# Kernel tuning notes

Measured on AMD Instinct MI355X. Metric: run time of the kernel, lower is better.

The kernel has to match this reference:

```python
import jax, jax.numpy as jnp
import numpy as np

TEMPERATURE = 0.1
B, T, D = 8, 1024, 1024
NEG_INF = -1e30

def setup_inputs() -> dict:
    key = jax.random.key(0)
    k1, k2, k3 = jax.random.split(key, 3)
    features = jax.random.normal(k1, (B, T, D), dtype=jnp.float32)
    masks = jax.random.bernoulli(k2, 0.05, (B, 1, T, T)).astype(jnp.float32)
    input_coords_length = jax.random.randint(k3, (B,), T // 2, T - 1)  # int32
    return {"features": features, "masks": masks, "input_coords_length": input_coords_length}


def _sup_con_loss(feat, mask, L):
    # feat: [T, D], mask: [T, T] float, L: scalar int valid length (slice [:L, :L])
    Tn = feat.shape[0]
    dt = feat.dtype
    vr = jnp.arange(Tn) < L                              # valid rows/cols [T]
    valid2d = (vr[:, None] & vr[None, :]).astype(dt)     # [T, T]
    dot = jnp.matmul(feat, feat.T) / TEMPERATURE         # [T, T]
    dot = jnp.where(vr[None, :], dot, NEG_INF)           # exclude padded cols from max
    logits = dot - jax.lax.stop_gradient(jnp.max(dot, axis=-1, keepdims=True))
    logits_mask = (1.0 - jnp.eye(Tn, dtype=dt)) * valid2d  # off-diagonal, in-slice
    exp_logits = jnp.exp(logits) * logits_mask
    m = mask * valid2d
    # negative_mask = 1-mask; entries < 1 zeroed (binary mask -> indicator of mask==0)
    neg = 1.0 - m
    neg = jnp.where(neg < 1.0, 0.0, neg) * valid2d
    # positive_mask = mask with entries > 0 set to 1
    pos = jnp.where(m > 0, 1.0, m)
    neg_denom = jnp.sum(exp_logits * neg, axis=-1, keepdims=True)
    pos_denom = jax.lax.stop_gradient(jnp.sum(exp_logits * pos, axis=-1, keepdims=True))
    log_prob = logits - jnp.log(neg_denom + pos_denom + 1e-6)
    m2 = m * logits_mask
    mean_log_prob_pos = (m2 * log_prob).sum(-1) / (m2.sum(-1) + 1e-6)  # [T]
    # mean over the L valid rows only (matches .mean() on the sliced tensor)
    return -jnp.sum(jnp.where(vr, mean_log_prob_pos, 0.0)) / L.astype(dt)


def _is_valid(mask, L):
    # valid sample iff sliced mask differs from eye(L) with [0,0]=0
    Tn = mask.shape[0]
    vr = jnp.arange(Tn) < L
    valid2d = (vr[:, None] & vr[None, :]).astype(mask.dtype)
    sanity = jnp.eye(Tn, dtype=mask.dtype).at[0, 0].set(0.0) * valid2d
    return jnp.any((mask * valid2d) != sanity)


def reference(features, masks, input_coords_length):
    L = input_coords_length + 1                      # [B]
    mask0 = masks[:, 0]                              # [B, T, T] (num_layers asserted == 1)
    losses = jax.vmap(_sup_con_loss)(features, mask0, L)   # [B]
    valid = jax.vmap(_is_valid)(mask0, L)                  # [B] bool
    vbs = jnp.maximum(jnp.sum(valid.astype(features.dtype)), 1.0)
    return jnp.sum(losses) / vbs
```

## Files before the change

kernel.cpp:

```cpp
#include <hip/hip_runtime.h>
#include <hip/hip_bf16.h>
#include <stdint.h>

#define T_DIM 1024
#define B_DIM 8

typedef __attribute__((ext_vector_type(8))) short short8;
typedef __attribute__((ext_vector_type(4))) float f32x4;

__device__ inline void gll16(const void* g, void* l) {
  __builtin_amdgcn_global_load_lds((__attribute__((address_space(1))) void*)g,
                                   (__attribute__((address_space(3))) void*)l,
                                   16, 0, 0);
}

__global__ __launch_bounds__(256) void convert_kernel(const float* __restrict__ F,
                                                      __hip_bfloat16* __restrict__ Fb) {
  const int t = blockIdx.x * 256 + threadIdx.x;
  const float4 v = ((const float4*)F)[t];
  union { __hip_bfloat16 h[4]; uint64_t u; } p;
  p.h[0] = __float2bfloat16(v.x);
  p.h[1] = __float2bfloat16(v.y);
  p.h[2] = __float2bfloat16(v.z);
  p.h[3] = __float2bfloat16(v.w);
  ((uint64_t*)Fb)[t] = p.u;
}

__global__ __launch_bounds__(512) void fused_kernel(const __hip_bfloat16* __restrict__ Fb,
                                                    const float* __restrict__ M,
                                                    const int* __restrict__ icl,
                                                    float* __restrict__ part) {
  const int b  = blockIdx.z;
  const int rt = blockIdx.y;
  const int ct = blockIdx.x;
  const int L  = icl[b] + 1;
  if (rt * 128 >= L || ct * 128 >= L) return;

  __shared__ __hip_bfloat16 As[2][4096];
  __shared__ __hip_bfloat16 Bs[2][4096];
  __shared__ float rp_m[128][4], rp_d[128][4], rp_s[128][4], rp_c[128][4], rp_b[128][4];

  const __hip_bfloat16* F = Fb + ((size_t)b << 20);
  const int tid  = threadIdx.x;
  const int lane = tid & 63;
  const int wave = tid >> 6;
  const int wrow = (wave >> 2) * 64;
  const int wcol = (wave & 3) * 32;
  const int row0 = rt * 128;
  const int col0 = ct * 128;
  const bool diag = (rt == ct);

  const int fr = lane & 15;
  const int q  = lane >> 4;
  const int fk = q * 8;

  const int sr = tid >> 2;
  const int sk = (tid & 3) * 8;

  f32x4 acc[4][2];
#pragma unroll
  for (int i = 0; i < 4; i++)
#pragma unroll
    for (int j = 0; j < 2; j++) acc[i][j] = (f32x4){0.f, 0.f, 0.f, 0.f};

  for (int k0 = 0; k0 < T_DIM; k0 += 64) {
    __syncthreads();
    gll16(F + (size_t)(row0 + sr) * T_DIM + k0 + sk,      &As[0][tid * 8]);
    gll16(F + (size_t)(row0 + sr) * T_DIM + k0 + 32 + sk, &As[1][tid * 8]);
    if (!diag) {
      gll16(F + (size_t)(col0 + sr) * T_DIM + k0 + sk,      &Bs[0][tid * 8]);
      gll16(F + (size_t)(col0 + sr) * T_DIM + k0 + 32 + sk, &Bs[1][tid * 8]);
    }
    __syncthreads();
#pragma unroll
    for (int kk = 0; kk < 2; kk++) {
      const __hip_bfloat16* Ab = As[kk];
      const __hip_bfloat16* Bb = diag ? As[kk] : Bs[kk];
      short8 af[4], bfr[2];
#pragma unroll
      for (int t = 0; t < 4; t++)
        af[t] = *(const short8*)(Ab + (wrow + t * 16 + fr) * 32 + fk);
#pragma unroll
      for (int j = 0; j < 2; j++)
        bfr[j] = *(const short8*)(Bb + (wcol + j * 16 + fr) * 32 + fk);
#pragma unroll
      for (int ti = 0; ti < 4; ti++)
#pragma unroll
        for (int tj = 0; tj < 2; tj++)
          acc[ti][tj] = __builtin_amdgcn_mfma_f32_16x16x32_bf16(af[ti], bfr[tj], acc[ti][tj], 0, 0, 0);
    }
  }

  const float* Mb = M + ((size_t)b << 20);
  const int gc0 = col0 + wcol + fr;
  const int gc1 = gc0 + 16;
#pragma unroll
  for (int ti = 0; ti < 4; ti++) {
#pragma unroll
    for (int r = 0; r < 4; r++) {
      const int lrow = wrow + ti * 16 + q * 4 + r;
      const int grow = row0 + lrow;
      const float s0 = (gc0 < L) ? acc[ti][0][r] * 10.0f : -1e30f;
      const float s1 = (gc1 < L) ? acc[ti][1][r] * 10.0f : -1e30f;
      float m = fmaxf(s0, s1);
#pragma unroll
      for (int d = 1; d < 16; d <<= 1) m = fmaxf(m, __shfl_xor(m, d, 64));
      float den = 0.f, msum = 0.f, cnt = 0.f, badf = 0.f;
      if (gc0 < L) {
        const float mk = Mb[(size_t)grow * T_DIM + gc0];
        if (gc0 != grow) { den += __expf(s0 - m); msum += mk * s0; cnt += mk; }
        const float sane = (gc0 == grow && grow != 0) ? 1.f : 0.f;
        badf = fmaxf(badf, (mk != sane) ? 1.f : 0.f);
      }
      if (gc1 < L) {
        const float mk = Mb[(size_t)grow * T_DIM + gc1];
        if (gc1 != grow) { den += __expf(s1 - m); msum += mk * s1; cnt += mk; }
        const float sane = (gc1 == grow && grow != 0) ? 1.f : 0.f;
        badf = fmaxf(badf, (mk != sane) ? 1.f : 0.f);
      }
#pragma unroll
      for (int d = 1; d < 16; d <<= 1) {
        den  += __shfl_xor(den, d, 64);
        msum += __shfl_xor(msum, d, 64);
        cnt  += __shfl_xor(cnt, d, 64);
        badf  = fmaxf(badf, __shfl_xor(badf, d, 64));
      }
      if (fr == 0) {
        const int slot = wave & 3;
        rp_m[lrow][slot] = m;   rp_d[lrow][slot] = den;
        rp_s[lrow][slot] = msum; rp_c[lrow][slot] = cnt;
        rp_b[lrow][slot] = badf;
      }
    }
  }
  __syncthreads();

  if (tid < 128) {
    float m = -1e30f;
#pragma unroll
    for (int s = 0; s < 4; s++) m = fmaxf(m, rp_m[tid][s]);
    float den = 0.f, msum = 0.f, cnt = 0.f, badf = 0.f;
#pragma unroll
    for (int s = 0; s < 4; s++) {
      den  += rp_d[tid][s] * __expf(rp_m[tid][s] - m);
      msum += rp_s[tid][s];
      cnt  += rp_c[tid][s];
      badf  = fmaxf(badf, rp_b[tid][s]);
    }
    float* p = part + ((((size_t)b * 1024 + row0 + tid) * 8) + ct) * 5;
    p[0] = m; p[1] = den; p[2] = msum; p[3] = cnt; p[4] = badf;
  }
}

__global__ __launch_bounds__(256) void reduce_kernel(const float* __restrict__ part,
                                                     const int* __restrict__ icl,
                                                     float* __restrict__ blk_sum,
                                                     int* __restrict__ blk_bad) {
  const int blk = blockIdx.x;
  const int row = blk * 256 + threadIdx.x;
  const int b = row >> 10;
  const int i = row & 1023;
  const int L = icl[b] + 1;
  float rv = 0.f;
  int bad = 0;
  if (i < L) {
    const float* p = part + (size_t)row * 40;
    const int ns = (L + 127) >> 7;
    float m = -1e30f;
    for (int s = 0; s < ns; s++) m = fmaxf(m, p[s * 5 + 0]);
    float den = 0.f, msum = 0.f, cnt = 0.f, badf = 0.f;
    for (int s = 0; s < ns; s++) {
      den  += p[s * 5 + 1] * __expf(p[s * 5 + 0] - m);
      msum += p[s * 5 + 2];
      cnt  += p[s * 5 + 3];
      badf  = fmaxf(badf, p[s * 5 + 4]);
    }
    const float A = msum - cnt * m;
    const float mlpp = (A - cnt * __logf(den + 1e-6f)) / (cnt + 1e-6f);
    rv = -mlpp / (float)L;
    bad = badf > 0.f ? 1 : 0;
  }
  const int tid  = threadIdx.x;
  const int lane = tid & 63;
  const int wave = tid >> 6;
  for (int o = 32; o > 0; o >>= 1) rv += __shfl_down(rv, o, 64);
  const int wbad = (__ballot(bad) != 0ull) ? 1 : 0;
  __shared__ float sred[4];
  __shared__ int bred[4];
  if (lane == 0) { sred[wave] = rv; bred[wave] = wbad; }
  __syncthreads();
  if (tid == 0) {
    blk_sum[blk] = sred[0] + sred[1] + sred[2] + sred[3];
    blk_bad[blk] = bred[0] | bred[1] | bred[2] | bred[3];
  }
}

__global__ __launch_bounds__(64) void final_kernel(const float* __restrict__ blk_sum,
                                                   const int* __restrict__ blk_bad,
                                                   float* __restrict__ out) {
  const int tid = threadIdx.x;
  float v = (tid < 32) ? blk_sum[tid] : 0.f;
  for (int o = 32; o > 0; o >>= 1) v += __shfl_down(v, o, 64);
  if (tid == 0) {
    int vcount = 0;
    for (int bb = 0; bb < B_DIM; bb++) {
      const int any = blk_bad[bb * 4] | blk_bad[bb * 4 + 1] |
                      blk_bad[bb * 4 + 2] | blk_bad[bb * 4 + 3];
      vcount += any ? 1 : 0;
    }
    out[0] = v / fmaxf((float)vcount, 1.0f);
  }
}

extern "C" void kernel_launch(void* const* d_in, const int* in_sizes, int n_in,
                              void* d_out, int out_size, void* d_ws, size_t ws_size,
                              hipStream_t stream) {
  const float* feat = (const float*)d_in[0];
  const float* mask = (const float*)d_in[1];
  const int*   icl  = (const int*)d_in[2];
  float* out = (float*)d_out;

  char* ws = (char*)d_ws;
  __hip_bfloat16* Fb = (__hip_bfloat16*)ws;
  float* part    = (float*)(ws + (16u << 20));
  float* blk_sum = (float*)(ws + (18u << 20));
  int*   blk_bad = (int*)(ws + (18u << 20) + 512);

  convert_kernel<<<dim3(8192), dim3(256), 0, stream>>>(feat, Fb);
  fused_kernel<<<dim3(8, 8, 8), dim3(512), 0, stream>>>(Fb, mask, icl, part);
  reduce_kernel<<<dim3(32), dim3(256), 0, stream>>>(part, icl, blk_sum, blk_bad);
  final_kernel<<<dim3(1), dim3(64), 0, stream>>>(blk_sum, blk_bad, out);
}
```

Before: 138.5 us.

## Double K-step per barrier, XOR-swizzle LDS, alias epilogue scratch, prefetch mask loads

Each loop iteration now loads 128 K-elements into four 32-wide LDS slabs, which halves the number of barrier pairs. An XOR swizzle on the 16-byte chunk index is applied both to the global source address and to the fragment read offset, to cut LDS bank conflicts on fragment reads. The reduction scratch now aliases the tile buffers in a single 64KB shared array, which needs an extra barrier after the main loop. The mask loads for each 16-row group are issued together before the reduction math so their global latency overlaps. The larger LDS footprint may lower occupancy.

```diff
diff --git a/kernel.cpp b/kernel.cpp
--- a/kernel.cpp
+++ b/kernel.cpp
@@ -36,9 +36,15 @@
   const int L  = icl[b] + 1;
   if (rt * 128 >= L || ct * 128 >= L) return;
 
-  __shared__ __hip_bfloat16 As[2][4096];
-  __shared__ __hip_bfloat16 Bs[2][4096];
-  __shared__ float rp_m[128][4], rp_d[128][4], rp_s[128][4], rp_c[128][4], rp_b[128][4];
+  __shared__ char smem[65536];
+  __hip_bfloat16* As = (__hip_bfloat16*)smem;
+  __hip_bfloat16* Bs = (__hip_bfloat16*)(smem + 32768);
+  float* rp = (float*)smem;
+  float* rp_m = rp;
+  float* rp_d = rp + 512;
+  float* rp_s = rp + 1024;
+  float* rp_c = rp + 1536;
+  float* rp_b = rp + 2048;
 
   const __hip_bfloat16* F = Fb + ((size_t)b << 20);
   const int tid  = threadIdx.x;
@@ -52,10 +58,10 @@
 
   const int fr = lane & 15;
   const int q  = lane >> 4;
-  const int fk = q * 8;
-
-  const int sr = tid >> 2;
-  const int sk = (tid & 3) * 8;
+  const int sl8 = (q ^ ((fr >> 1) & 3)) * 8;
+
+  const int srow = tid >> 2;
+  const int sgk  = (((tid & 3) ^ ((tid >> 3) & 3)) * 8);
 
   f32x4 acc[4][2];
 #pragma unroll
@@ -63,26 +69,30 @@
 #pragma unroll
     for (int j = 0; j < 2; j++) acc[i][j] = (f32x4){0.f, 0.f, 0.f, 0.f};
 
-  for (int k0 = 0; k0 < T_DIM; k0 += 64) {
+  for (int k0 = 0; k0 < T_DIM; k0 += 128) {
     __syncthreads();
-    gll16(F + (size_t)(row0 + sr) * T_DIM + k0 + sk,      &As[0][tid * 8]);
-    gll16(F + (size_t)(row0 + sr) * T_DIM + k0 + 32 + sk, &As[1][tid * 8]);
+#pragma unroll
+    for (int p = 0; p < 4; p++)
+      gll16(F + (size_t)(row0 + srow) * T_DIM + k0 + p * 32 + sgk,
+            As + p * 4096 + tid * 8);
     if (!diag) {
-      gll16(F + (size_t)(col0 + sr) * T_DIM + k0 + sk,      &Bs[0][tid * 8]);
-      gll16(F + (size_t)(col0 + sr) * T_DIM + k0 + 32 + sk, &Bs[1][tid * 8]);
+#pragma unroll
+      for (int p = 0; p < 4; p++)
+        gll16(F + (size_t)(col0 + srow) * T_DIM + k0 + p * 32 + sgk,
+              Bs + p * 4096 + tid * 8);
     }
     __syncthreads();
 #pragma unroll
-    for (int kk = 0; kk < 2; kk++) {
-      const __hip_bfloat16* Ab = As[kk];
-      const __hip_bfloat16* Bb = diag ? As[kk] : Bs[kk];
+    for (int kk = 0; kk < 4; kk++) {
+      const __hip_bfloat16* Ab = As + kk * 4096;
+      const __hip_bfloat16* Bb = diag ? Ab : (Bs + kk * 4096);
       short8 af[4], bfr[2];
 #pragma unroll
       for (int t = 0; t < 4; t++)
-        af[t] = *(const short8*)(Ab + (wrow + t * 16 + fr) * 32 + fk);
+        af[t] = *(const short8*)(Ab + (wrow + t * 16 + fr) * 32 + sl8);
 #pragma unroll
       for (int j = 0; j < 2; j++)
-        bfr[j] = *(const short8*)(Bb + (wcol + j * 16 + fr) * 32 + fk);
+        bfr[j] = *(const short8*)(Bb + (wcol + j * 16 + fr) * 32 + sl8);
 #pragma unroll
       for (int ti = 0; ti < 4; ti++)
 #pragma unroll
@@ -90,12 +100,20 @@
           acc[ti][tj] = __builtin_amdgcn_mfma_f32_16x16x32_bf16(af[ti], bfr[tj], acc[ti][tj], 0, 0, 0);
     }
   }
+  __syncthreads();
 
   const float* Mb = M + ((size_t)b << 20);
   const int gc0 = col0 + wcol + fr;
   const int gc1 = gc0 + 16;
 #pragma unroll
   for (int ti = 0; ti < 4; ti++) {
+    float mk0[4], mk1[4];
+#pragma unroll
+    for (int r = 0; r < 4; r++) {
+      const int grow = row0 + wrow + ti * 16 + q * 4 + r;
+      mk0[r] = (gc0 < L) ? Mb[(size_t)grow * T_DIM + gc0] : 0.f;
+      mk1[r] = (gc1 < L) ? Mb[(size_t)grow * T_DIM + gc1] : 0.f;
+    }
 #pragma unroll
     for (int r = 0; r < 4; r++) {
       const int lrow = wrow + ti * 16 + q * 4 + r;
@@ -107,16 +125,14 @@
       for (int d = 1; d < 16; d <<= 1) m = fmaxf(m, __shfl_xor(m, d, 64));
       float den = 0.f, msum = 0.f, cnt = 0.f, badf = 0.f;
       if (gc0 < L) {
-        const float mk = Mb[(size_t)grow * T_DIM + gc0];
-        if (gc0 != grow) { den += __expf(s0 - m); msum += mk * s0; cnt += mk; }
+        if (gc0 != grow) { den += __expf(s0 - m); msum += mk0[r] * s0; cnt += mk0[r]; }
         const float sane = (gc0 == grow && grow != 0) ? 1.f : 0.f;
-        badf = fmaxf(badf, (mk != sane) ? 1.f : 0.f);
+        badf = fmaxf(badf, (mk0[r] != sane) ? 1.f : 0.f);
       }
       if (gc1 < L) {
-        const float mk = Mb[(size_t)grow * T_DIM + gc1];
-        if (gc1 != grow) { den += __expf(s1 - m); msum += mk * s1; cnt += mk; }
+        if (gc1 != grow) { den += __expf(s1 - m); msum += mk1[r] * s1; cnt += mk1[r]; }
         const float sane = (gc1 == grow && grow != 0) ? 1.f : 0.f;
-        badf = fmaxf(badf, (mk != sane) ? 1.f : 0.f);
+        badf = fmaxf(badf, (mk1[r] != sane) ? 1.f : 0.f);
       }
 #pragma unroll
       for (int d = 1; d < 16; d <<= 1) {
@@ -127,9 +143,9 @@
       }
       if (fr == 0) {
         const int slot = wave & 3;
-        rp_m[lrow][slot] = m;   rp_d[lrow][slot] = den;
-        rp_s[lrow][slot] = msum; rp_c[lrow][slot] = cnt;
-        rp_b[lrow][slot] = badf;
+        rp_m[lrow * 4 + slot] = m;   rp_d[lrow * 4 + slot] = den;
+        rp_s[lrow * 4 + slot] = msum; rp_c[lrow * 4 + slot] = cnt;
+        rp_b[lrow * 4 + slot] = badf;
       }
     }
   }
@@ -138,14 +154,14 @@
   if (tid < 128) {
     float m = -1e30f;
 #pragma unroll
-    for (int s = 0; s < 4; s++) m = fmaxf(m, rp_m[tid][s]);
+    for (int s = 0; s < 4; s++) m = fmaxf(m, rp_m[tid * 4 + s]);
     float den = 0.f, msum = 0.f, cnt = 0.f, badf = 0.f;
 #pragma unroll
     for (int s = 0; s < 4; s++) {
-      den  += rp_d[tid][s] * __expf(rp_m[tid][s] - m);
-      msum += rp_s[tid][s];
-      cnt  += rp_c[tid][s];
-      badf  = fmaxf(badf, rp_b[tid][s]);
+      den  += rp_d[tid * 4 + s] * __expf(rp_m[tid * 4 + s] - m);
+      msum += rp_s[tid * 4 + s];
+      cnt  += rp_c[tid * 4 + s];
+      badf  = fmaxf(badf, rp_b[tid * 4 + s]);
     }
     float* p = part + ((((size_t)b * 1024 + row0 + tid) * 8) + ct) * 5;
     p[0] = m; p[1] = den; p[2] = msum; p[3] = cnt; p[4] = badf;
```

New measurement: 134.0 us. 3.2% less time.
